# Kernel tuning notes

Measured on AMD Instinct MI355X. Metric: run time of the kernel, lower is better.

Reference implementation:

```python
import jax, jax.numpy as jnp
import numpy as np

N_HEAD, D_MODEL, D_HEAD = 16, 1024, 64
QLEN, MLEN, BSZ = 1024, 1024, 4
KLEN = QLEN + MLEN
RLEN = KLEN
LN_EPS = 1e-5


def setup_inputs() -> dict:
    key = jax.random.key(0)
    ks = jax.random.split(key, 12)
    s = 0.02
    query = jax.random.normal(ks[0], (QLEN, BSZ, D_MODEL), jnp.float32)
    content = jax.random.normal(ks[1], (QLEN, BSZ, D_MODEL), jnp.float32)
    mems = jax.random.normal(ks[2], (MLEN, BSZ, D_MODEL), jnp.float32)
    r = jax.random.normal(ks[3], (RLEN, D_MODEL), jnp.float32)
    # causal mask with memory offset: query i may attend keys j <= i + MLEN
    i = jnp.arange(QLEN)[:, None]
    j = jnp.arange(KLEN)[None, :]
    attn_mask = (j > i + MLEN)[:, :, None]  # [qlen, klen, 1] bool, True = masked
    Wq = jax.random.normal(ks[4], (D_MODEL, N_HEAD * D_HEAD), jnp.float32) * s
    Wk = jax.random.normal(ks[5], (D_MODEL, N_HEAD * D_HEAD), jnp.float32) * s
    Wv = jax.random.normal(ks[6], (D_MODEL, N_HEAD * D_HEAD), jnp.float32) * s
    Wr = jax.random.normal(ks[7], (D_MODEL, N_HEAD * D_HEAD), jnp.float32) * s
    Wo = jax.random.normal(ks[8], (N_HEAD * D_HEAD, D_MODEL), jnp.float32) * s
    r_w_bias = jax.random.normal(ks[9], (N_HEAD, D_HEAD), jnp.float32) * s
    r_r_bias = jax.random.normal(ks[10], (N_HEAD, D_HEAD), jnp.float32) * s
    ln_gamma = jnp.ones((D_MODEL,), jnp.float32)
    ln_beta = jnp.zeros((D_MODEL,), jnp.float32)
    return dict(query=query, content=content, r=r, mems=mems, attn_mask=attn_mask,
                Wq=Wq, Wk=Wk, Wv=Wv, Wr=Wr, Wo=Wo,
                r_w_bias=r_w_bias, r_r_bias=r_r_bias,
                ln_gamma=ln_gamma, ln_beta=ln_beta)


def _rel_shift(x, cut_len):
    # x: [qlen, rlen, bsz, n_head]
    q, rl, b, n = x.shape
    zero_pad = jnp.zeros((q, 1, b, n), x.dtype)
    xp = jnp.concatenate([zero_pad, x], axis=1)          # [q, rl+1, b, n]
    xp = xp.reshape(rl + 1, q, b, n)[1:].reshape(q, rl, b, n)
    return xp[:, :cut_len]


def _layer_norm(x, gamma, beta):
    mu = jnp.mean(x, axis=-1, keepdims=True)
    var = jnp.mean(jnp.square(x - mu), axis=-1, keepdims=True)
    return (x - mu) * jax.lax.rsqrt(var + LN_EPS) * gamma + beta


def reference(query, content, r, mems, attn_mask, Wq, Wk, Wv, Wr, Wo,
              r_w_bias, r_r_bias, ln_gamma, ln_beta):
    qlen, bsz = query.shape[0], query.shape[1]
    cat = jnp.concatenate([mems, content], axis=0)        # [klen, b, d_model]
    klen = cat.shape[0]
    scale = 1.0 / (D_HEAD ** 0.5)

    w_head_q = (query @ Wq).reshape(qlen, bsz, N_HEAD, D_HEAD)
    w_head_k = (cat @ Wk).reshape(klen, bsz, N_HEAD, D_HEAD)
    w_head_v = (cat @ Wv).reshape(klen, bsz, N_HEAD, D_HEAD)
    r_head_k = (r @ Wr).reshape(-1, N_HEAD, D_HEAD)       # [rlen, n, d]

    AC = jnp.einsum('ibnd,jbnd->ijbn', w_head_q + r_w_bias, w_head_k)
    BD = jnp.einsum('ibnd,jnd->ijbn', w_head_q + r_r_bias, r_head_k)
    BD = _rel_shift(BD, cut_len=klen)

    attn_score = (AC + BD) * scale                        # [q, k, b, n]
    attn_score = jnp.where(attn_mask[:, :, :, None], jnp.float32(-1e30), attn_score)
    attn_prob = jax.nn.softmax(attn_score, axis=1)

    attn_vec = jnp.einsum('ijbn,jbnd->ibnd', attn_prob, w_head_v)
    attn_vec = attn_vec.reshape(qlen, bsz, N_HEAD * D_HEAD)
    attn_out = attn_vec @ Wo                              # [q, b, d_model]

    out = _layer_norm(query + attn_out, ln_gamma, ln_beta)
    return out
```

## Files before the change

### kernel.cpp

```cpp
#include <hip/hip_runtime.h>
#include <cstdint>
#include <cstddef>

constexpr int QLEN = 1024, MLEN = 1024, KLEN = 2048, RLEN = 2048;
constexpr int BSZ = 4, NH = 16, DH = 64, DM = 1024;

typedef __attribute__((ext_vector_type(8))) short bf16x8_t;
typedef __attribute__((ext_vector_type(4))) float f32x4_t;

#define DEV __device__ __forceinline__

DEV float b2f(unsigned short u) {
    union { unsigned x; float f; } v; v.x = ((unsigned)u) << 16; return v.f;
}
DEV unsigned short f2b(float f) {
    unsigned x = __float_as_uint(f);
    unsigned r = (x + 0x7fffu + ((x >> 16) & 1u)) >> 16;
    return (unsigned short)r;
}
DEV unsigned pack2(float lo, float hi) {
    return (unsigned)f2b(lo) | ((unsigned)f2b(hi) << 16);
}
DEV unsigned cvtpk(float lo, float hi) {
    unsigned r;
    asm("v_cvt_pk_bf16_f32 %0, %1, %2" : "=v"(r) : "v"(lo), "v"(hi));
    return r;
}
DEV void gl16(const unsigned short* g, unsigned short* l) {
    __builtin_amdgcn_global_load_lds(
        (const __attribute__((address_space(1))) unsigned int*)(const void*)g,
        (__attribute__((address_space(3))) unsigned int*)(void*)l, 16, 0, 0);
}

__global__ __launch_bounds__(256) void conv_bf16(const float* __restrict__ q,
                                                 const float* __restrict__ mems,
                                                 const float* __restrict__ content,
                                                 unsigned short* __restrict__ Qb,
                                                 unsigned short* __restrict__ catb) {
    const int which = blockIdx.y;
    const float* s = which == 0 ? q : (which == 1 ? mems : content);
    unsigned short* d = which == 0 ? Qb : (which == 1 ? catb : catb + (size_t)4096 * DM);
    size_t i = ((size_t)blockIdx.x * 256 + threadIdx.x) * 8;
    float4 f0 = *(const float4*)(s + i);
    float4 f1 = *(const float4*)(s + i + 4);
    uint4 pk;
    pk.x = pack2(f0.x, f0.y); pk.y = pack2(f0.z, f0.w);
    pk.z = pack2(f1.x, f1.y); pk.w = pack2(f1.z, f1.w);
    *(uint4*)(d + i) = pk;
}

__global__ __launch_bounds__(256) void transW_all(const float* __restrict__ Wq,
                                                  const float* __restrict__ Wk,
                                                  const float* __restrict__ Wv,
                                                  const float* __restrict__ Wr,
                                                  const float* __restrict__ Wo,
                                                  unsigned short* __restrict__ WqT,
                                                  unsigned short* __restrict__ WkvT,
                                                  unsigned short* __restrict__ WrT,
                                                  unsigned short* __restrict__ WoT) {
    const int z = blockIdx.z;
    const float* W = z == 0 ? Wq : z == 1 ? Wk : z == 2 ? Wv : z == 3 ? Wr : Wo;
    unsigned short* WT = z == 0 ? WqT : z == 1 ? WkvT
                       : z == 2 ? WkvT + (size_t)1024 * 1024 : z == 3 ? WrT : WoT;
    __shared__ float t[32][33];
    const int tx = threadIdx.x & 31, ty = threadIdx.x >> 5;
    const int n0 = blockIdx.x * 32, k0 = blockIdx.y * 32;
#pragma unroll
    for (int r = 0; r < 32; r += 8)
        t[ty + r][tx] = W[(size_t)(k0 + ty + r) * DM + n0 + tx];
    __syncthreads();
#pragma unroll
    for (int r = 0; r < 32; r += 8)
        WT[(size_t)(n0 + ty + r) * DM + k0 + tx] = f2b(t[tx][ty + r]);
}

__global__ __launch_bounds__(256) void gemm_proj(const unsigned short* __restrict__ Qb,
                                                 const unsigned short* __restrict__ catb,
                                                 const float* __restrict__ r_in,
                                                 const unsigned short* __restrict__ WqT,
                                                 const unsigned short* __restrict__ WkvT,
                                                 const unsigned short* __restrict__ WrT,
                                                 unsigned short* __restrict__ Qp,
                                                 unsigned short* __restrict__ Kp,
                                                 unsigned short* __restrict__ VT,
                                                 unsigned short* __restrict__ Rp) {
    constexpr int K = DM;
    const int bx = blockIdx.x;
    int seg, loc, gx;
    const unsigned short* BT;
    if (bx < 256)       { seg = 0; loc = bx;        gx = 8;  BT = WqT; }
    else if (bx < 1280) { seg = 1; loc = bx - 256;  gx = 16; BT = WkvT; }
    else                { seg = 2; loc = bx - 1280; gx = 8;  BT = WrT; }
    const int m0 = (loc / gx) * 128, n0 = (loc % gx) * 128;
    const bool isV = (seg == 1) && (n0 >= 1024);
    const int vb = m0 >> 11, vj0 = m0 & 2047;

    __shared__ unsigned short As[128 * 64];
    __shared__ unsigned short Bs[128 * 64];

    const int tid = threadIdx.x;
    const int wave = tid >> 6, lane = tid & 63;
    const int quad = lane >> 4, l16 = lane & 15;
    const int wm = (wave >> 1) * 64, wn = (wave & 1) * 64;
    const int ls = lane >> 3, l8 = lane & 7;
    const int sg = l8 ^ ls;
    const int swz7 = l16 & 7;

    const unsigned short* abase = (seg == 0) ? Qb : catb;

    f32x4_t acc[4][4] = {};

    for (int it = 0; it < K / 64; it++) {
        const int k0 = it * 64;

#pragma unroll
        for (int c = 0; c < 4; c++) {
            int cb = wave * 4 + c;
            int row = cb * 8 + ls;
            gl16(BT + (size_t)(n0 + row) * K + k0 + sg * 8, &Bs[cb * 512]);
        }
        if (seg != 2) {
#pragma unroll
            for (int c = 0; c < 4; c++) {
                int ca = wave * 4 + c;
                int row = ca * 8 + ls;
                size_t ar = isV ? (size_t)((vj0 + row) * 4 + vb) * K
                                : (size_t)(m0 + row) * K;
                gl16(abase + ar + k0 + sg * 8, &As[ca * 512]);
            }
        } else {
            const int srow = tid >> 1, hk = tid & 1;
            const float* ap = r_in + (size_t)(m0 + srow) * K + k0 + hk * 32;
#pragma unroll
            for (int c = 0; c < 4; c++) {
                float4 f0 = *(const float4*)(ap + c * 8);
                float4 f1 = *(const float4*)(ap + c * 8 + 4);
                uint4 pk;
                pk.x = pack2(f0.x, f0.y); pk.y = pack2(f0.z, f0.w);
                pk.z = pack2(f1.x, f1.y); pk.w = pack2(f1.z, f1.w);
                int slot = (hk * 4 + c) ^ (srow & 7);
                *(uint4*)((char*)As + srow * 128 + slot * 16) = pk;
            }
        }
        __syncthreads();

#pragma unroll
        for (int h = 0; h < 2; h++) {
            bf16x8_t af[4], bfr[4];
#pragma unroll
            for (int s = 0; s < 4; s++) {
                int arow = wm + s * 16 + l16;
                int brow = wn + s * 16 + l16;
                af[s]  = *(const bf16x8_t*)((const char*)As + arow * 128 + (((h * 4 + quad) ^ swz7) << 4));
                bfr[s] = *(const bf16x8_t*)((const char*)Bs + brow * 128 + (((h * 4 + quad) ^ swz7) << 4));
            }
#pragma unroll
            for (int sm = 0; sm < 4; sm++)
#pragma unroll
                for (int sn = 0; sn < 4; sn++)
                    acc[sm][sn] = __builtin_amdgcn_mfma_f32_16x16x32_bf16(af[sm], bfr[sn], acc[sm][sn], 0, 0, 0);
        }
        __syncthreads();
    }

#pragma unroll
    for (int sm = 0; sm < 4; sm++)
#pragma unroll
        for (int sn = 0; sn < 4; sn++) {
            if (isV) {
                int j = vj0 + wm + sm * 16 + quad * 4;
                int d = (n0 - 1024) + wn + sn * 16 + l16;
                uint2 pk;
                pk.x = pack2(acc[sm][sn][0], acc[sm][sn][1]);
                pk.y = pack2(acc[sm][sn][2], acc[sm][sn][3]);
                *(uint2*)(VT + ((size_t)(vb * DM + d)) * KLEN + j) = pk;
            } else {
#pragma unroll
                for (int rg = 0; rg < 4; rg++) {
                    int row = m0 + wm + sm * 16 + quad * 4 + rg;
                    int col = n0 + wn + sn * 16 + l16;
                    unsigned short v = f2b(acc[sm][sn][rg]);
                    if (seg == 0)      Qp[(size_t)row * 1024 + col] = v;
                    else if (seg == 2) Rp[(size_t)row * 1024 + col] = v;
                    else               Kp[(size_t)row * 1024 + col] = v;
                }
            }
        }
}

__global__ __launch_bounds__(256) void attn_flash(const unsigned short* __restrict__ Qp,
                                                  const unsigned short* __restrict__ Kp,
                                                  const unsigned short* __restrict__ VT,
                                                  const unsigned short* __restrict__ Rp,
                                                  const float* __restrict__ rwb,
                                                  const float* __restrict__ rrb,
                                                  unsigned short* __restrict__ O0,
                                                  unsigned short* __restrict__ O1,
                                                  float* __restrict__ lsum) {
    const int n = blockIdx.x, b = blockIdx.y;
    const int s = blockIdx.z & 1;
    const int i0 = (7 - (blockIdx.z >> 1)) * 128;
    const int tid = threadIdx.x;
    const int wave = tid >> 6, lane = tid & 63;
    const int l16 = lane & 15, quad = lane >> 4;
    const int ib = i0 + wave * 32;

    __shared__ unsigned short kvr[320 * 64];
    __shared__ unsigned short sbuf[4][2][16 * 88];

    const int swz = (l16 & 7) * 8;
    const int soA = (quad * 8) ^ swz;
    const int soB = (quad * 8 + 32) ^ swz;

    const int lrow8 = lane >> 3;
    const int sg8 = ((lane & 7) ^ lrow8) * 8;
    unsigned short* const stg = &kvr[(wave * 80) << 6];

    const float SCL = 0.18033688011112042f;

    bf16x8_t qac[2][2], qbd[2][2];
#pragma unroll
    for (int g = 0; g < 2; g++) {
        const unsigned short* qrow = Qp + ((size_t)((ib + g * 16 + l16) * BSZ + b)) * DM + n * DH;
#pragma unroll
        for (int kb = 0; kb < 2; kb++) {
            int off = kb * 32 + quad * 8;
            union { uint4 u4; unsigned short us[8]; } in;
            in.u4 = *(const uint4*)(qrow + off);
            union { bf16x8_t v; unsigned short us[8]; } oa, ob;
#pragma unroll
            for (int t = 0; t < 8; t++) {
                float q = b2f(in.us[t]);
                oa.us[t] = f2b((q + rwb[n * DH + off + t]) * SCL);
                ob.us[t] = f2b((q + rrb[n * DH + off + t]) * SCL);
            }
            qac[g][kb] = oa.v; qbd[g][kb] = ob.v;
        }
    }

    f32x4_t accO[2][4] = {};
    float l_i[2][4] = {};

    const unsigned short* const vsrc0 = VT + ((size_t)(b * DM + n * DH)) * KLEN;
    const unsigned short* const rsrc0 = Rp + n * DH;

    const int jtB = ((i0 + 96 + 31 + MLEN) >> 6) + 1;
    for (int jt = s; jt < jtB; jt += 2) {
        const int jb = jt * 64;
        const int pmin = jb - i0 + 896;

#pragma unroll
        for (int i = 0; i < 10; i++) {
            const int row = wave * 80 + i * 8 + lrow8;
            const unsigned short* src;
            if (row < 64) {
                src = Kp + ((size_t)((jb + row) * BSZ + b)) * DM + n * DH + sg8;
            } else if (row < 128) {
                src = vsrc0 + (size_t)(row - 64) * KLEN + jb + sg8;
            } else {
                src = rsrc0 + (size_t)(pmin + row - 128) * DM + sg8;
            }
            gl16(src, stg + (i << 9));
        }
        __syncthreads();

        if (jb <= ib + 31 + MLEN) {
            const int pb_rel = 96 - 32 * wave;

#pragma unroll
            for (int h = 0; h < 2; h++) {
                f32x4_t accB[2][3] = {};
#pragma unroll
                for (int t3 = 0; t3 < 3; t3++) {
                    int rrow = 128 + pb_rel + (h * 3 + t3) * 16 + l16;
                    bf16x8_t r0 = *(const bf16x8_t*)&kvr[(rrow << 6) + soA];
                    bf16x8_t r1 = *(const bf16x8_t*)&kvr[(rrow << 6) + soB];
                    accB[0][t3] = __builtin_amdgcn_mfma_f32_16x16x32_bf16(qbd[0][0], r0, accB[0][t3], 0, 0, 0);
                    accB[0][t3] = __builtin_amdgcn_mfma_f32_16x16x32_bf16(qbd[0][1], r1, accB[0][t3], 0, 0, 0);
                    accB[1][t3] = __builtin_amdgcn_mfma_f32_16x16x32_bf16(qbd[1][0], r0, accB[1][t3], 0, 0, 0);
                    accB[1][t3] = __builtin_amdgcn_mfma_f32_16x16x32_bf16(qbd[1][1], r1, accB[1][t3], 0, 0, 0);
                }
#pragma unroll
                for (int t3 = 0; t3 < 3; t3++) {
                    int t = h * 3 + t3;
                    int rowb = quad * 4;
#pragma unroll
                    for (int g = 0; g < 2; g++) {
                        if (g == 0 ? (t >= 1) : (t <= 4)) {
                            unsigned lo = cvtpk(accB[g][t3][0], accB[g][t3][1]);
                            unsigned hi = cvtpk(accB[g][t3][2], accB[g][t3][3]);
                            int base = (g == 0 ? (t - 1) : t) * 16 + l16;
                            sbuf[wave][g][(rowb + 0) * 88 + base] = (unsigned short)lo;
                            sbuf[wave][g][(rowb + 1) * 88 + base] = (unsigned short)(lo >> 16);
                            sbuf[wave][g][(rowb + 2) * 88 + base] = (unsigned short)hi;
                            sbuf[wave][g][(rowb + 3) * 88 + base] = (unsigned short)(hi >> 16);
                        }
                    }
                }
            }

            float pprev[2][4];
#pragma unroll
            for (int nt = 0; nt < 4; nt++) {
                int krow = nt * 16 + l16;
                bf16x8_t k0 = *(const bf16x8_t*)&kvr[(krow << 6) + soA];
                bf16x8_t k1 = *(const bf16x8_t*)&kvr[(krow << 6) + soB];
                f32x4_t aS0 = {}, aS1 = {};
                aS0 = __builtin_amdgcn_mfma_f32_16x16x32_bf16(qac[0][0], k0, aS0, 0, 0, 0);
                aS0 = __builtin_amdgcn_mfma_f32_16x16x32_bf16(qac[0][1], k1, aS0, 0, 0, 0);
                aS1 = __builtin_amdgcn_mfma_f32_16x16x32_bf16(qac[1][0], k0, aS1, 0, 0, 0);
                aS1 = __builtin_amdgcn_mfma_f32_16x16x32_bf16(qac[1][1], k1, aS1, 0, 0, 0);

                if (nt > 0) {
                    int col = (nt - 1) * 16 + l16, rowb = quad * 4;
#pragma unroll
                    for (int g = 0; g < 2; g++) {
                        unsigned lo = cvtpk(pprev[g][0], pprev[g][1]);
                        unsigned hi = cvtpk(pprev[g][2], pprev[g][3]);
                        sbuf[wave][g][(rowb + 0) * 88 + col] = (unsigned short)lo;
                        sbuf[wave][g][(rowb + 1) * 88 + col] = (unsigned short)(lo >> 16);
                        sbuf[wave][g][(rowb + 2) * 88 + col] = (unsigned short)hi;
                        sbuf[wave][g][(rowb + 3) * 88 + col] = (unsigned short)(hi >> 16);
                    }
                }

                if (jb + 63 <= ib + MLEN) {
#pragma unroll
                    for (int g = 0; g < 2; g++)
#pragma unroll
                        for (int r = 0; r < 4; r++) {
                            int irow = quad * 4 + r;
                            float sc = (g ? aS1 : aS0)[r]
                                     + b2f(sbuf[wave][g][irow * 88 + nt * 16 + l16 - irow + 15]);
                            float e = __builtin_amdgcn_exp2f(sc);
                            l_i[g][r] += e;
                            pprev[g][r] = e;
                        }
                } else {
#pragma unroll
                    for (int g = 0; g < 2; g++)
#pragma unroll
                        for (int r = 0; r < 4; r++) {
                            int irow = quad * 4 + r;
                            float sc = (g ? aS1 : aS0)[r]
                                     + b2f(sbuf[wave][g][irow * 88 + nt * 16 + l16 - irow + 15]);
                            bool ok = (jb + nt * 16 + l16) <= (ib + g * 16 + irow + MLEN);
                            float e = ok ? __builtin_amdgcn_exp2f(sc) : 0.f;
                            l_i[g][r] += e;
                            pprev[g][r] = e;
                        }
                }
            }
            {
                int col = 48 + l16, rowb = quad * 4;
#pragma unroll
                for (int g = 0; g < 2; g++) {
                    unsigned lo = cvtpk(pprev[g][0], pprev[g][1]);
                    unsigned hi = cvtpk(pprev[g][2], pprev[g][3]);
                    sbuf[wave][g][(rowb + 0) * 88 + col] = (unsigned short)lo;
                    sbuf[wave][g][(rowb + 1) * 88 + col] = (unsigned short)(lo >> 16);
                    sbuf[wave][g][(rowb + 2) * 88 + col] = (unsigned short)hi;
                    sbuf[wave][g][(rowb + 3) * 88 + col] = (unsigned short)(hi >> 16);
                }
            }

#pragma unroll
            for (int kb2 = 0; kb2 < 2; kb2++) {
                bf16x8_t pf0 = *(const bf16x8_t*)&sbuf[wave][0][l16 * 88 + kb2 * 32 + quad * 8];
                bf16x8_t pf1 = *(const bf16x8_t*)&sbuf[wave][1][l16 * 88 + kb2 * 32 + quad * 8];
#pragma unroll
                for (int nt = 0; nt < 4; nt++) {
                    int vrow = 64 + nt * 16 + l16;
                    bf16x8_t vf = *(const bf16x8_t*)&kvr[(vrow << 6) + (kb2 ? soB : soA)];
                    accO[0][nt] = __builtin_amdgcn_mfma_f32_16x16x32_bf16(pf0, vf, accO[0][nt], 0, 0, 0);
                    accO[1][nt] = __builtin_amdgcn_mfma_f32_16x16x32_bf16(pf1, vf, accO[1][nt], 0, 0, 0);
                }
            }
        }
        __syncthreads();
    }

#pragma unroll
    for (int g = 0; g < 2; g++)
#pragma unroll
        for (int r = 0; r < 4; r++)
#pragma unroll
            for (int off = 1; off < 16; off <<= 1)
                l_i[g][r] += __shfl_xor(l_i[g][r], off);

    unsigned short* Op = s ? O1 : O0;
#pragma unroll
    for (int g = 0; g < 2; g++)
#pragma unroll
        for (int r = 0; r < 4; r++) {
            int irow = ib + g * 16 + quad * 4 + r;
            int rowlin = irow * BSZ + b;
            unsigned short* orow = Op + (size_t)rowlin * DM + n * DH;
#pragma unroll
            for (int nt = 0; nt < 4; nt++)
                orow[nt * 16 + l16] = f2b(accO[g][nt][r]);
            if (l16 == 0)
                lsum[((size_t)(s * 4096) + rowlin) * NH + n] = l_i[g][r];
        }
}

__global__ __launch_bounds__(256) void merge_part(const unsigned short* __restrict__ O0,
                                                  const unsigned short* __restrict__ O1,
                                                  const float* __restrict__ lsum,
                                                  unsigned short* __restrict__ AV) {
    const int row = blockIdx.x;
    const int d = threadIdx.x * 4;
    const int n = d >> 6;
    float l0 = lsum[(size_t)row * NH + n];
    float l1 = lsum[((size_t)4096 + row) * NH + n];
    float inv = 1.0f / (l0 + l1);
    size_t idx = (size_t)row * DM + d;
    unsigned short a[4], bb[4], res[4];
    *(uint2*)a  = *(const uint2*)(O0 + idx);
    *(uint2*)bb = *(const uint2*)(O1 + idx);
#pragma unroll
    for (int k = 0; k < 4; k++) res[k] = f2b((b2f(a[k]) + b2f(bb[k])) * inv);
    *(uint2*)(AV + idx) = *(uint2*)res;
}

__global__ __launch_bounds__(256) void gemm_wo(const unsigned short* __restrict__ A,
                                               const unsigned short* __restrict__ BT,
                                               unsigned short* __restrict__ C) {
    constexpr int K = DM, N = DM;
    __shared__ unsigned short As[128 * 64];
    __shared__ unsigned short Bs[64 * 64];

    const int tid = threadIdx.x;
    const int wave = tid >> 6, lane = tid & 63;
    const int quad = lane >> 4, l16 = lane & 15;
    const int m0 = blockIdx.y * 128, n0 = blockIdx.x * 64;
    const int wm = (wave >> 1) * 64, wn = (wave & 1) * 32;
    const int ls = lane >> 3, l8 = lane & 7;
    const int sg = l8 ^ ls;
    const int swz7 = l16 & 7;

    f32x4_t acc[4][2] = {};

    for (int it = 0; it < K / 64; it++) {
        const int k0 = it * 64;

#pragma unroll
        for (int c = 0; c < 4; c++) {
            int rb = wave * 32 + c * 8;
            gl16(A + (size_t)(m0 + rb + ls) * K + k0 + sg * 8, &As[rb * 64]);
        }
#pragma unroll
        for (int c = 0; c < 2; c++) {
            int rb = wave * 16 + c * 8;
            gl16(BT + (size_t)(n0 + rb + ls) * K + k0 + sg * 8, &Bs[rb * 64]);
        }
        __syncthreads();

#pragma unroll
        for (int h = 0; h < 2; h++) {
            bf16x8_t af[4], bfr[2];
#pragma unroll
            for (int s = 0; s < 4; s++)
                af[s] = *(const bf16x8_t*)((const char*)As + (wm + s * 16 + l16) * 128 + (((h * 4 + quad) ^ swz7) << 4));
#pragma unroll
            for (int s = 0; s < 2; s++)
                bfr[s] = *(const bf16x8_t*)((const char*)Bs + (wn + s * 16 + l16) * 128 + (((h * 4 + quad) ^ swz7) << 4));
#pragma unroll
            for (int sm = 0; sm < 4; sm++)
#pragma unroll
                for (int sn = 0; sn < 2; sn++)
                    acc[sm][sn] = __builtin_amdgcn_mfma_f32_16x16x32_bf16(af[sm], bfr[sn], acc[sm][sn], 0, 0, 0);
        }
        __syncthreads();
    }

#pragma unroll
    for (int sm = 0; sm < 4; sm++)
#pragma unroll
        for (int sn = 0; sn < 2; sn++)
#pragma unroll
            for (int rg = 0; rg < 4; rg++) {
                int row = m0 + wm + sm * 16 + quad * 4 + rg;
                int col = n0 + wn + sn * 16 + l16;
                C[(size_t)row * N + col] = f2b(acc[sm][sn][rg]);
            }
}

__global__ __launch_bounds__(256) void ln_kernel(const float* __restrict__ query,
                                                 const unsigned short* __restrict__ AO,
                                                 const float* __restrict__ gamma,
                                                 const float* __restrict__ beta,
                                                 float* __restrict__ out) {
    const int row = blockIdx.x;
    const int tid = threadIdx.x;
    __shared__ float redS[4], redQ[4];

    float x[4], s = 0.f, ss = 0.f;
#pragma unroll
    for (int c = 0; c < 4; c++) {
        int d = c * 256 + tid;
        float v = query[(size_t)row * DM + d] + b2f(AO[(size_t)row * DM + d]);
        x[c] = v; s += v; ss += v * v;
    }
#pragma unroll
    for (int off = 32; off; off >>= 1) { s += __shfl_xor(s, off); ss += __shfl_xor(ss, off); }
    int w = tid >> 6, lane = tid & 63;
    if (lane == 0) { redS[w] = s; redQ[w] = ss; }
    __syncthreads();
    s  = redS[0] + redS[1] + redS[2] + redS[3];
    ss = redQ[0] + redQ[1] + redQ[2] + redQ[3];
    float mu  = s * (1.0f / DM);
    float var = ss * (1.0f / DM) - mu * mu;
    float inv = rsqrtf(var + 1e-5f);
#pragma unroll
    for (int c = 0; c < 4; c++) {
        int d = c * 256 + tid;
        out[(size_t)row * DM + d] = (x[c] - mu) * inv * gamma[d] + beta[d];
    }
}

extern "C" void kernel_launch(void* const* d_in, const int* in_sizes, int n_in,
                              void* d_out, int out_size, void* d_ws, size_t ws_size,
                              hipStream_t stream) {
    const float* query   = (const float*)d_in[0];
    const float* content = (const float*)d_in[1];
    const float* r_in    = (const float*)d_in[2];
    const float* mems    = (const float*)d_in[3];
    const float* Wq  = (const float*)d_in[5];
    const float* Wk  = (const float*)d_in[6];
    const float* Wv  = (const float*)d_in[7];
    const float* Wr  = (const float*)d_in[8];
    const float* Wo  = (const float*)d_in[9];
    const float* rwb = (const float*)d_in[10];
    const float* rrb = (const float*)d_in[11];
    const float* gam = (const float*)d_in[12];
    const float* bet = (const float*)d_in[13];
    float* out = (float*)d_out;

    char* ws = (char*)d_ws;
    unsigned short* WqT  = (unsigned short*)(ws);
    unsigned short* WkvT = (unsigned short*)(ws + (2u  << 20));
    unsigned short* WrT  = (unsigned short*)(ws + (6u  << 20));
    unsigned short* WoT  = (unsigned short*)(ws + (8u  << 20));
    unsigned short* Qp   = (unsigned short*)(ws + (10u << 20));
    unsigned short* Kp   = (unsigned short*)(ws + (18u << 20));
    unsigned short* VT   = (unsigned short*)(ws + (34u << 20));
    unsigned short* Rp   = (unsigned short*)(ws + (50u << 20));
    unsigned short* Qb   = (unsigned short*)(ws + (54u << 20));
    float*          lsum = (float*)(ws);
    unsigned short* AV   = (unsigned short*)(ws + (10u << 20));
    unsigned short* AO   = (unsigned short*)(ws);

    unsigned short* catb = (unsigned short*)d_out;
    unsigned short* O0   = (unsigned short*)d_out;
    unsigned short* O1   = (unsigned short*)d_out + (size_t)4096 * DM;

    conv_bf16<<<dim3(2048, 3), 256, 0, stream>>>(query, mems, content, Qb, catb);
    transW_all<<<dim3(32, 32, 5), 256, 0, stream>>>(Wq, Wk, Wv, Wr, Wo,
                                                    WqT, WkvT, WrT, WoT);

    gemm_proj<<<dim3(1408), 256, 0, stream>>>(Qb, catb, r_in, WqT, WkvT, WrT,
                                              Qp, Kp, VT, Rp);

    attn_flash<<<dim3(NH, BSZ, 16), 256, 0, stream>>>(Qp, Kp, VT, Rp, rwb, rrb,
                                                      O0, O1, lsum);

    merge_part<<<dim3(4096), 256, 0, stream>>>(O0, O1, lsum, AV);
    gemm_wo<<<dim3(16, 32), 256, 0, stream>>>(AV, WoT, AO);
    ln_kernel<<<dim3(4096), 256, 0, stream>>>(query, AO, gam, bet, out);
}
```

Measured before the change: 340.4 us.

## Prefetch next K/V/R tile into registers to overlap global loads with compute

Replaces the direct global-to-LDS loads (gl16) of each K/V/R tile with a register-staged software pipeline. The next iteration's tile is loaded into registers while the current tile is being computed, then written to shared memory with an XOR swizzle at the top of the following iteration. This is meant to hide global memory latency behind the MFMA work. The cost is ten extra uint4 registers per thread, which may reduce occupancy, plus explicit LDS store instructions.

```diff
diff --git a/kernel.cpp b/kernel.cpp
--- a/kernel.cpp
+++ b/kernel.cpp
@@ -212,9 +212,8 @@
     const int soA = (quad * 8) ^ swz;
     const int soB = (quad * 8 + 32) ^ swz;
 
-    const int lrow8 = lane >> 3;
-    const int sg8 = ((lane & 7) ^ lrow8) * 8;
-    unsigned short* const stg = &kvr[(wave * 80) << 6];
+    const int str = tid >> 3, sslot = tid & 7;
+    const int wso = (sslot ^ (str & 7)) * 8;
 
     const float SCL = 0.18033688011112042f;
 
@@ -241,28 +240,41 @@
     f32x4_t accO[2][4] = {};
     float l_i[2][4] = {};
 
-    const unsigned short* const vsrc0 = VT + ((size_t)(b * DM + n * DH)) * KLEN;
-    const unsigned short* const rsrc0 = Rp + n * DH;
+    const unsigned short* const vsrc0 = VT + ((size_t)(b * DM + n * DH)) * KLEN + sslot * 8;
+    const unsigned short* const rsrc0 = Rp + n * DH + sslot * 8;
+
+    uint4 rgs[10];
+    auto loadstage = [&](int jt2) {
+        const int jb2 = jt2 * 64;
+        const int pmin2 = jb2 - i0 + 896;
+#pragma unroll
+        for (int c = 0; c < 10; c++) {
+            const int row = c * 32 + str;
+            const unsigned short* src;
+            if (c < 2) {
+                src = Kp + ((size_t)((jb2 + row) * BSZ + b)) * DM + n * DH + sslot * 8;
+            } else if (c < 4) {
+                src = vsrc0 + (size_t)(row - 64) * KLEN + jb2;
+            } else {
+                src = rsrc0 + (size_t)(pmin2 + row - 128) * DM;
+            }
+            rgs[c] = *(const uint4*)src;
+        }
+    };
 
     const int jtB = ((i0 + 96 + 31 + MLEN) >> 6) + 1;
+    loadstage(s);
     for (int jt = s; jt < jtB; jt += 2) {
         const int jb = jt * 64;
-        const int pmin = jb - i0 + 896;
-
-#pragma unroll
-        for (int i = 0; i < 10; i++) {
-            const int row = wave * 80 + i * 8 + lrow8;
-            const unsigned short* src;
-            if (row < 64) {
-                src = Kp + ((size_t)((jb + row) * BSZ + b)) * DM + n * DH + sg8;
-            } else if (row < 128) {
-                src = vsrc0 + (size_t)(row - 64) * KLEN + jb + sg8;
-            } else {
-                src = rsrc0 + (size_t)(pmin + row - 128) * DM + sg8;
-            }
-            gl16(src, stg + (i << 9));
+
+#pragma unroll
+        for (int c = 0; c < 10; c++) {
+            const int row = c * 32 + str;
+            *(uint4*)&kvr[(row << 6) + wso] = rgs[c];
         }
         __syncthreads();
+
+        if (jt + 2 < jtB) loadstage(jt + 2);
 
         if (jb <= ib + 31 + MLEN) {
             const int pb_rel = 96 - 32 * wave;
```

After: 429.1 us. 26.1% more time.
